# Kernel tuning notes

Hardware: AMD Instinct MI355X
Metric: run time of the kernel (lower is better)

Reference implementation:

```python
import jax, jax.numpy as jnp
import numpy as np

B, N, D = 16, 4096, 256
S = 8            # num_slots
ITERS = 3
H = 256          # mlp hidden = max(dim, 256)
SCALE = D ** -0.5
TEMP = 1.0
LN_EPS = 1e-5


def _ln(x, g, b):
    mu = jnp.mean(x, axis=-1, keepdims=True)
    var = jnp.var(x, axis=-1, keepdims=True)
    return (x - mu) * jax.lax.rsqrt(var + LN_EPS) * g + b


def setup_inputs() -> dict:
    key = jax.random.key(0)
    ks = jax.random.split(key, 16)
    xav = float(np.sqrt(6.0 / (S * D + D)))  # xavier_uniform over (1,S,D)
    lin = float(np.sqrt(1.0 / D))
    return {
        "embeddings": jax.random.normal(ks[0], (B, N, D), jnp.float32),
        "slots_noise": jax.random.normal(ks[1], (1, S, D), jnp.float32) * 0.0 + jax.random.normal(ks[1], (B, S, D), jnp.float32),
        "slots_mu": jax.random.uniform(ks[2], (1, S, D), jnp.float32, -xav, xav),
        "slots_logsigma": jax.random.uniform(ks[3], (1, S, D), jnp.float32, -xav, xav),
        "Wk": jax.random.uniform(ks[4], (S, D, D), jnp.float32, -lin, lin),
        "Wq": jax.random.uniform(ks[5], (D, D), jnp.float32, -lin, lin),
        "Wv": jax.random.uniform(ks[6], (S, D, D), jnp.float32, -lin, lin),
        "W_ih": jax.random.uniform(ks[7], (3 * D, D), jnp.float32, -lin, lin),
        "W_hh": jax.random.uniform(ks[8], (3 * D, D), jnp.float32, -lin, lin),
        "b_ih": jax.random.uniform(ks[9], (3 * D,), jnp.float32, -lin, lin),
        "b_hh": jax.random.uniform(ks[10], (3 * D,), jnp.float32, -lin, lin),
        "W1": jax.random.uniform(ks[11], (H, D), jnp.float32, -lin, lin),
        "b1": jnp.zeros((H,), jnp.float32),
        "W2": jax.random.uniform(ks[12], (D, H), jnp.float32, -float(np.sqrt(1.0 / H)), float(np.sqrt(1.0 / H))),
        "b2": jnp.zeros((D,), jnp.float32),
        "g_in": jnp.ones((D,), jnp.float32), "be_in": jnp.zeros((D,), jnp.float32),
        "g_s": jnp.ones((D,), jnp.float32), "be_s": jnp.zeros((D,), jnp.float32),
        "g_ff": jnp.ones((D,), jnp.float32), "be_ff": jnp.zeros((D,), jnp.float32),
    }


def _gru(x, h, W_ih, W_hh, b_ih, b_hh):
    # torch.nn.GRUCell math; x,h: [M, D]
    gi = x @ W_ih.T + b_ih
    gh = h @ W_hh.T + b_hh
    i_r, i_z, i_n = jnp.split(gi, 3, axis=-1)
    h_r, h_z, h_n = jnp.split(gh, 3, axis=-1)
    r = jax.nn.sigmoid(i_r + h_r)
    z = jax.nn.sigmoid(i_z + h_z)
    n = jnp.tanh(i_n + r * h_n)
    return (1.0 - z) * n + z * h


def reference(embeddings, slots_noise, slots_mu, slots_logsigma, Wk, Wq, Wv,
              W_ih, W_hh, b_ih, b_hh, W1, b1, W2, b2,
              g_in, be_in, g_s, be_s, g_ff, be_ff):
    b, n, d = embeddings.shape
    slots = slots_mu + jnp.exp(slots_logsigma) * slots_noise   # [B,S,D]
    emb = _ln(embeddings, g_in, be_in)                          # [B,N,D]
    # per-slot keys / values: keys[s] = emb @ Wk[s].T  -> [S,B,N,D]
    keys = jnp.einsum('bnd,sed->sbne', emb, Wk)
    values = jnp.einsum('bnd,sed->sbne', emb, Wv)

    attn_vis = None
    for _ in range(ITERS):
        slots_prev = slots
        slots_n = _ln(slots, g_s, be_s)
        q = jnp.einsum('bsd,ed->bse', slots_n, Wq)              # [B,S,D]
        dots = jnp.einsum('bsd,sbnd->bsn', q, keys) * SCALE     # [B,S,N]
        attn = jax.nn.softmax(dots / TEMP, axis=1)              # softmax over slots
        attn_vis = attn
        attn_w = attn / jnp.sum(attn, axis=-1, keepdims=True)   # normalize over tokens
        updates = jnp.einsum('sbnd,bsn->bsd', values, attn_w)   # [B,S,D]
        h = _gru(updates.reshape(b * S, d), slots_prev.reshape(b * S, d),
                 W_ih, W_hh, b_ih, b_hh).reshape(b, S, d)
        ff = _ln(h, g_ff, be_ff)
        slots = h + (jax.nn.relu(ff @ W1.T + b1) @ W2.T + b2)
    return slots, attn_vis
```

## Files before the change

### kernel.cpp

```cpp
#include <hip/hip_runtime.h>

#define DEVI __device__ __forceinline__

constexpr float SCALE = 0.0625f;
constexpr float LN_EPS = 1e-5f;

DEVI float dot8f(const float* __restrict__ w, const float* __restrict__ x){
  float4 a = *(const float4*)w;
  float4 b = *(const float4*)(w + 4);
  return a.x*x[0]+a.y*x[1]+a.z*x[2]+a.w*x[3]+b.x*x[4]+b.y*x[5]+b.z*x[6]+b.w*x[7];
}

DEVI float gemv256(const float* __restrict__ W, const float* __restrict__ xv,
                   float (*part)[33], int tid){
  const int c8 = tid & 31, dp = tid >> 5;
  float xs8[8];
  #pragma unroll
  for (int j = 0; j < 8; ++j) xs8[j] = xv[c8*8 + j];
  #pragma unroll 4
  for (int di = 0; di < 32; ++di){
    int d = dp*32 + di;
    part[d][c8] = dot8f(W + (size_t)d*256 + c8*8, xs8);
  }
  __syncthreads();
  float acc = 0.f;
  #pragma unroll
  for (int p = 0; p < 32; ++p) acc += part[tid][p];
  __syncthreads();
  return acc;
}

DEVI float block_ln(float x, const float* __restrict__ g, const float* __restrict__ be,
                    float* red, int tid, int lane, int wv){
  float v1 = x, v2 = x*x;
  #pragma unroll
  for (int o = 32; o; o >>= 1){ v1 += __shfl_xor(v1,o,64); v2 += __shfl_xor(v2,o,64); }
  if (lane == 0){ red[wv] = v1; red[4+wv] = v2; }
  __syncthreads();
  float mu = (red[0]+red[1]+red[2]+red[3]) * (1.f/256.f);
  float var = (red[4]+red[5]+red[6]+red[7]) * (1.f/256.f) - mu*mu;
  float inv = rsqrtf(var + LN_EPS);
  float r = (x - mu)*inv*g[tid] + be[tid];
  __syncthreads();
  return r;
}

DEVI void q_gen(float snew, int r, int s, int tid, int lane, int wv,
                const float* __restrict__ Wq, const float* __restrict__ Wk,
                const float* __restrict__ g_s, const float* __restrict__ be_s,
                const float* __restrict__ g_in, const float* __restrict__ be_in,
                float* __restrict__ qg, float* __restrict__ gqbq,
                float* xv, float (*part)[33], float (*partK)[256], float* red){
  float sn = block_ln(snew, g_s, be_s, red, tid, lane, wv);
  xv[tid] = sn; __syncthreads();
  float q = gemv256(Wq, xv, part, tid);
  xv[tid] = q; __syncthreads();
  const int c8 = tid & 31, ep = tid >> 5;
  float acc8[8];
  #pragma unroll
  for (int j = 0; j < 8; ++j) acc8[j] = 0.f;
  const float* Wb = Wk + ((size_t)s*256)*256 + c8*8;
  #pragma unroll 4
  for (int ei = 0; ei < 32; ++ei){
    int e = ep*32 + ei;
    const float* wp = Wb + (size_t)e*256;
    float4 wa = *(const float4*)wp;
    float4 wb = *(const float4*)(wp + 4);
    float qe = xv[e];
    acc8[0] += qe*wa.x; acc8[1] += qe*wa.y; acc8[2] += qe*wa.z; acc8[3] += qe*wa.w;
    acc8[4] += qe*wb.x; acc8[5] += qe*wb.y; acc8[6] += qe*wb.z; acc8[7] += qe*wb.w;
  }
  float* pk = &partK[ep][c8*8];
  #pragma unroll
  for (int j = 0; j < 8; ++j) pk[j] = acc8[j];
  __syncthreads();
  float qk = 0.f;
  #pragma unroll
  for (int p = 0; p < 8; ++p) qk += partK[p][tid];
  float qgv = qk * g_in[tid] * SCALE;
  float bqv = qk * be_in[tid] * SCALE;
  qg[r*256 + tid] = qgv;
  float vq = qgv, vb = bqv;
  #pragma unroll
  for (int o = 32; o; o >>= 1){ vq += __shfl_xor(vq,o,64); vb += __shfl_xor(vb,o,64); }
  if (lane == 0){ red[wv] = vq; red[4+wv] = vb; }
  __syncthreads();
  if (tid == 0) gqbq[r*2+0] = red[0]+red[1]+red[2]+red[3];
  if (tid == 1) gqbq[r*2+1] = red[4]+red[5]+red[6]+red[7];
}

__global__ __launch_bounds__(256) void k_qg0(const float* __restrict__ noise,
    const float* __restrict__ smu, const float* __restrict__ slsig,
    const float* __restrict__ Wq, const float* __restrict__ Wk,
    const float* __restrict__ g_s, const float* __restrict__ be_s,
    const float* __restrict__ g_in, const float* __restrict__ be_in,
    float* __restrict__ slots, float* __restrict__ qg, float* __restrict__ gqbq,
    float* __restrict__ uacc, float* __restrict__ Zacc){
  __shared__ float part[256][33];
  __shared__ float partK[8][256];
  __shared__ float xv[256];
  __shared__ float red[8];
  const int r = blockIdx.x, tid = threadIdx.x;
  const int s = r & 7, lane = tid & 63, wv = tid >> 6;
  float x = smu[s*256 + tid] + expf(slsig[s*256 + tid]) * noise[r*256 + tid];
  slots[r*256 + tid] = x;
  uacc[r*256 + tid] = 0.f;
  if (tid == 0) Zacc[r] = 0.f;
  q_gen(x, r, s, tid, lane, wv, Wq, Wk, g_s, be_s, g_in, be_in, qg, gqbq,
        xv, part, partK, red);
}

__global__ __launch_bounds__(256) void k_main(const float* __restrict__ emb,
    const float* __restrict__ qg, const float* __restrict__ gqbq,
    const float* __restrict__ g_in, const float* __restrict__ be_in,
    float* __restrict__ uacc, float* __restrict__ Zacc,
    float* __restrict__ out_attn, int write_attn){
  __shared__ float qgL[2048];
  __shared__ float aL[256], avL[256];
  __shared__ float Wred[2][8][4];
  __shared__ float Zs[8], A2s[8], GqL[8], BqL[8];

  const int tid = threadIdx.x, lane = tid & 63, wv = tid >> 6;
  const int blk = blockIdx.x, b = blk >> 7, tile = blk & 127;
  const int n0 = tile * 32;

  {
    const float4* src = (const float4*)(qg + (size_t)b * 2048);
    float4* dst = (float4*)qgL;
    #pragma unroll
    for (int k = 0; k < 2; ++k){
      int w = tid + k*256;
      int s = w >> 6, f = w & 63, qq = f >> 3, j = f & 7;
      dst[s*64 + qq*8 + ((j + qq) & 7)] = src[w];
    }
  }
  if (tid < 8){
    GqL[tid] = gqbq[(b*8 + tid)*2 + 0];
    BqL[tid] = gqbq[(b*8 + tid)*2 + 1];
  }
  __syncthreads();

  const int t = tid >> 3;
  const int qq = tid & 7;
  {
    const float4* xrow = (const float4*)(emb + ((size_t)(b*4096 + n0 + t))*256 + qq*32);
    float4 xv4[8];
    #pragma unroll
    for (int j = 0; j < 8; ++j) xv4[j] = xrow[j];
    float s1 = 0.f, s2 = 0.f, acc[8];
    #pragma unroll
    for (int s = 0; s < 8; ++s) acc[s] = 0.f;
    #pragma unroll
    for (int j = 0; j < 8; ++j){
      float4 u = xv4[j];
      s1 += (u.x+u.y)+(u.z+u.w);
      s2 += u.x*u.x+u.y*u.y+u.z*u.z+u.w*u.w;
      const float* qb = qgL + qq*32 + ((j + qq) & 7)*4;
      #pragma unroll
      for (int s = 0; s < 8; ++s){
        float4 q0 = *(const float4*)(qb + s*256);
        acc[s] += u.x*q0.x + u.y*q0.y + u.z*q0.z + u.w*q0.w;
      }
    }
    #pragma unroll
    for (int o = 1; o <= 4; o <<= 1){
      s1 += __shfl_xor(s1,o,64); s2 += __shfl_xor(s2,o,64);
      #pragma unroll
      for (int s = 0; s < 8; ++s) acc[s] += __shfl_xor(acc[s],o,64);
    }
    float mu = s1 * (1.f/256.f);
    float var = s2 * (1.f/256.f) - mu*mu;
    float inv = rsqrtf(var + LN_EPS);
    float dv[8], mx = -1e30f;
    #pragma unroll
    for (int s = 0; s < 8; ++s){
      dv[s] = inv * (acc[s] - mu * GqL[s]) + BqL[s];
      mx = fmaxf(mx, dv[s]);
    }
    float den = 0.f;
    #pragma unroll
    for (int s = 0; s < 8; ++s){ dv[s] = expf(dv[s] - mx); den += dv[s]; }
    float rden = 1.f / den;
    #pragma unroll
    for (int s = 0; s < 8; ++s){
      float at = dv[s] * rden;
      float av = at * inv;
      if (qq == 0){ avL[s*32 + t] = at; aL[s*32 + t] = av; }
      float z1 = at, z2 = av * mu;
      #pragma unroll
      for (int o = 32; o; o >>= 1){ z1 += __shfl_xor(z1, o, 64); z2 += __shfl_xor(z2, o, 64); }
      if (lane == 0){ Wred[0][s][wv] = z1 * 0.125f; Wred[1][s][wv] = z2 * 0.125f; }
    }
  }
  __syncthreads();
  if (tid < 8){
    Zs[tid]  = Wred[0][tid][0]+Wred[0][tid][1]+Wred[0][tid][2]+Wred[0][tid][3];
    A2s[tid] = Wred[1][tid][0]+Wred[1][tid][1]+Wred[1][tid][2]+Wred[1][tid][3];
  }
  if (write_attn){
    int s = tid >> 5, tk = tid & 31;
    out_attn[((size_t)(b*8 + s))*4096 + n0 + tk] = avL[s*32 + tk];
  }
  __syncthreads();
  {
    const int c = tid;
    const float* xcol = emb + ((size_t)(b*4096 + n0))*256 + c;
    float S1[8];
    #pragma unroll
    for (int s = 0; s < 8; ++s) S1[s] = 0.f;
    #pragma unroll 2
    for (int t4 = 0; t4 < 8; ++t4){
      float x0 = xcol[(t4*4+0)*256];
      float x1 = xcol[(t4*4+1)*256];
      float x2 = xcol[(t4*4+2)*256];
      float x3 = xcol[(t4*4+3)*256];
      #pragma unroll
      for (int s = 0; s < 8; ++s){
        float4 a4 = *(const float4*)(&aL[s*32 + t4*4]);
        S1[s] += x0*a4.x + x1*a4.y + x2*a4.z + x3*a4.w;
      }
    }
    float gc = g_in[c], bc = be_in[c];
    float* dst = uacc + ((size_t)b*8)*256 + c;
    #pragma unroll
    for (int s = 0; s < 8; ++s){
      atomicAdd(&dst[s*256], gc * (S1[s] - A2s[s]) + bc * Zs[s]);
    }
    if (tid < 8) atomicAdd(&Zacc[b*8 + tid], Zs[tid]);
  }
}

__global__ __launch_bounds__(256) void k_fused(
    float* __restrict__ slots, float* __restrict__ uacc, float* __restrict__ Zacc,
    const float* __restrict__ Wv,
    const float* __restrict__ W_ih, const float* __restrict__ W_hh,
    const float* __restrict__ b_ih, const float* __restrict__ b_hh,
    const float* __restrict__ W1, const float* __restrict__ b1,
    const float* __restrict__ W2, const float* __restrict__ b2,
    const float* __restrict__ g_ff, const float* __restrict__ be_ff,
    const float* __restrict__ Wq, const float* __restrict__ Wk,
    const float* __restrict__ g_s, const float* __restrict__ be_s,
    const float* __restrict__ g_in, const float* __restrict__ be_in,
    float* __restrict__ qg, float* __restrict__ gqbq,
    float* __restrict__ out_slots, int last){
  __shared__ float part[256][33];
  __shared__ float partK[8][256];
  __shared__ float xv[256];
  __shared__ float red[8];
  __shared__ float zsh;
  const int r = blockIdx.x, tid = threadIdx.x;
  const int s = r & 7, lane = tid & 63, wv = tid >> 6;

  float u = uacc[r*256 + tid];
  uacc[r*256 + tid] = 0.f;
  if (tid == 0){ zsh = Zacc[r]; Zacc[r] = 0.f; }
  xv[tid] = u;
  __syncthreads();
  const float rz = 1.f / zsh;
  float upd = gemv256(Wv + (size_t)s*65536, xv, part, tid) * rz;

  xv[tid] = upd; __syncthreads();
  float i_r = gemv256(W_ih,           xv, part, tid) + b_ih[tid];
  float i_z = gemv256(W_ih +  65536,  xv, part, tid) + b_ih[256 + tid];
  float i_n = gemv256(W_ih + 131072,  xv, part, tid) + b_ih[512 + tid];

  float hp = slots[r*256 + tid];
  xv[tid] = hp; __syncthreads();
  float h_r = gemv256(W_hh,           xv, part, tid) + b_hh[tid];
  float h_z = gemv256(W_hh +  65536,  xv, part, tid) + b_hh[256 + tid];
  float h_n = gemv256(W_hh + 131072,  xv, part, tid) + b_hh[512 + tid];

  float rg = 1.f/(1.f + expf(-(i_r + h_r)));
  float zg = 1.f/(1.f + expf(-(i_z + h_z)));
  float ng = tanhf(i_n + rg*h_n);
  float h  = (1.f - zg)*ng + zg*hp;

  float lnh = block_ln(h, g_ff, be_ff, red, tid, lane, wv);
  xv[tid] = lnh; __syncthreads();
  float hid = fmaxf(gemv256(W1, xv, part, tid) + b1[tid], 0.f);
  xv[tid] = hid; __syncthreads();
  float out = h + gemv256(W2, xv, part, tid) + b2[tid];
  slots[r*256 + tid] = out;
  if (last){
    out_slots[r*256 + tid] = out;
    return;
  }
  q_gen(out, r, s, tid, lane, wv, Wq, Wk, g_s, be_s, g_in, be_in, qg, gqbq,
        xv, part, partK, red);
}

extern "C" void kernel_launch(void* const* d_in, const int* in_sizes, int n_in,
                              void* d_out, int out_size, void* d_ws, size_t ws_size,
                              hipStream_t stream){
  const float* emb   = (const float*)d_in[0];
  const float* noise = (const float*)d_in[1];
  const float* smu   = (const float*)d_in[2];
  const float* slsig = (const float*)d_in[3];
  const float* Wk    = (const float*)d_in[4];
  const float* Wq    = (const float*)d_in[5];
  const float* Wv    = (const float*)d_in[6];
  const float* W_ih  = (const float*)d_in[7];
  const float* W_hh  = (const float*)d_in[8];
  const float* b_ih  = (const float*)d_in[9];
  const float* b_hh  = (const float*)d_in[10];
  const float* W1    = (const float*)d_in[11];
  const float* b1    = (const float*)d_in[12];
  const float* W2    = (const float*)d_in[13];
  const float* b2    = (const float*)d_in[14];
  const float* g_in  = (const float*)d_in[15];
  const float* be_in = (const float*)d_in[16];
  const float* g_s   = (const float*)d_in[17];
  const float* be_s  = (const float*)d_in[18];
  const float* g_ff  = (const float*)d_in[19];
  const float* be_ff = (const float*)d_in[20];

  float* ws    = (float*)d_ws;
  float* slots = ws;
  float* qg    = ws + 32768;
  float* gqbq  = ws + 65536;
  float* uacc  = ws + 65792;
  float* Zacc  = ws + 98560;

  float* out_slots = (float*)d_out;
  float* out_attn  = out_slots + 32768;
  const int has_attn = (out_size >= 32768 + 16*8*4096);

  k_qg0<<<dim3(128), dim3(256), 0, stream>>>(noise, smu, slsig, Wq, Wk,
      g_s, be_s, g_in, be_in, slots, qg, gqbq, uacc, Zacc);
  for (int it = 0; it < 3; ++it){
    int last = (it == 2);
    k_main<<<dim3(2048), dim3(256), 0, stream>>>(emb, qg, gqbq, g_in, be_in,
        uacc, Zacc, out_attn, last && has_attn);
    k_fused<<<dim3(128), dim3(256), 0, stream>>>(slots, uacc, Zacc, Wv,
        W_ih, W_hh, b_ih, b_hh, W1, b1, W2, b2, g_ff, be_ff,
        Wq, Wk, g_s, be_s, g_in, be_in, qg, gqbq, out_slots, last);
  }
}
```

Before: 383.2 us.

## Widen slot-update blocks to 1024 threads and double token tile in main kernel

The per-slot GRU/MLP/query kernels now run 1024-thread blocks, so each GEMV row slice is split across four times as many threads with guarded reductions. This targets the latency of the serial small-GEMV chain. The main attention kernel processes 64 tokens per block in two passes, halving the grid and the number of atomic adds to the update accumulators. Its weighted-sum step is restructured into float4 row-parallel partial sums reduced through shared memory, and the atomic target order is staggered per block to spread contention. The changes cost larger shared memory and more syncs per block.

```diff
diff --git a/kernel.cpp b/kernel.cpp
--- a/kernel.cpp
+++ b/kernel.cpp
@@ -11,58 +11,64 @@
   return a.x*x[0]+a.y*x[1]+a.z*x[2]+a.w*x[3]+b.x*x[4]+b.y*x[5]+b.z*x[6]+b.w*x[7];
 }
 
-DEVI float gemv256(const float* __restrict__ W, const float* __restrict__ xv,
-                   float (*part)[33], int tid){
+DEVI float gemv256_w(const float* __restrict__ W, const float* __restrict__ xv,
+                     float (*part)[33], int tid){
   const int c8 = tid & 31, dp = tid >> 5;
   float xs8[8];
   #pragma unroll
   for (int j = 0; j < 8; ++j) xs8[j] = xv[c8*8 + j];
-  #pragma unroll 4
-  for (int di = 0; di < 32; ++di){
-    int d = dp*32 + di;
+  #pragma unroll
+  for (int di = 0; di < 8; ++di){
+    int d = dp*8 + di;
     part[d][c8] = dot8f(W + (size_t)d*256 + c8*8, xs8);
   }
   __syncthreads();
   float acc = 0.f;
-  #pragma unroll
-  for (int p = 0; p < 32; ++p) acc += part[tid][p];
+  if (tid < 256){
+    #pragma unroll
+    for (int p = 0; p < 32; ++p) acc += part[tid][p];
+  }
   __syncthreads();
   return acc;
 }
 
-DEVI float block_ln(float x, const float* __restrict__ g, const float* __restrict__ be,
-                    float* red, int tid, int lane, int wv){
+DEVI float block_ln2(float x, const float* __restrict__ g, const float* __restrict__ be,
+                     float* red, int tid){
+  const int lane = tid & 63, wv = tid >> 6;
   float v1 = x, v2 = x*x;
   #pragma unroll
   for (int o = 32; o; o >>= 1){ v1 += __shfl_xor(v1,o,64); v2 += __shfl_xor(v2,o,64); }
-  if (lane == 0){ red[wv] = v1; red[4+wv] = v2; }
+  if (tid < 256 && lane == 0){ red[wv] = v1; red[4+wv] = v2; }
   __syncthreads();
   float mu = (red[0]+red[1]+red[2]+red[3]) * (1.f/256.f);
   float var = (red[4]+red[5]+red[6]+red[7]) * (1.f/256.f) - mu*mu;
   float inv = rsqrtf(var + LN_EPS);
-  float r = (x - mu)*inv*g[tid] + be[tid];
+  float r = 0.f;
+  if (tid < 256) r = (x - mu)*inv*g[tid] + be[tid];
   __syncthreads();
   return r;
 }
 
-DEVI void q_gen(float snew, int r, int s, int tid, int lane, int wv,
+DEVI void q_gen(float snew, int r, int s, int tid,
                 const float* __restrict__ Wq, const float* __restrict__ Wk,
                 const float* __restrict__ g_s, const float* __restrict__ be_s,
                 const float* __restrict__ g_in, const float* __restrict__ be_in,
                 float* __restrict__ qg, float* __restrict__ gqbq,
                 float* xv, float (*part)[33], float (*partK)[256], float* red){
-  float sn = block_ln(snew, g_s, be_s, red, tid, lane, wv);
-  xv[tid] = sn; __syncthreads();
-  float q = gemv256(Wq, xv, part, tid);
-  xv[tid] = q; __syncthreads();
+  float sn = block_ln2(snew, g_s, be_s, red, tid);
+  if (tid < 256) xv[tid] = sn;
+  __syncthreads();
+  float q = gemv256_w(Wq, xv, part, tid);
+  if (tid < 256) xv[tid] = q;
+  __syncthreads();
   const int c8 = tid & 31, ep = tid >> 5;
   float acc8[8];
   #pragma unroll
   for (int j = 0; j < 8; ++j) acc8[j] = 0.f;
   const float* Wb = Wk + ((size_t)s*256)*256 + c8*8;
-  #pragma unroll 4
-  for (int ei = 0; ei < 32; ++ei){
-    int e = ep*32 + ei;
+  #pragma unroll
+  for (int ei = 0; ei < 8; ++ei){
+    int e = ep*8 + ei;
     const float* wp = Wb + (size_t)e*256;
     float4 wa = *(const float4*)wp;
     float4 wb = *(const float4*)(wp + 4);
@@ -74,22 +80,25 @@
   #pragma unroll
   for (int j = 0; j < 8; ++j) pk[j] = acc8[j];
   __syncthreads();
-  float qk = 0.f;
-  #pragma unroll
-  for (int p = 0; p < 8; ++p) qk += partK[p][tid];
-  float qgv = qk * g_in[tid] * SCALE;
-  float bqv = qk * be_in[tid] * SCALE;
-  qg[r*256 + tid] = qgv;
-  float vq = qgv, vb = bqv;
+  float vq = 0.f, vb = 0.f;
+  if (tid < 256){
+    float qk = 0.f;
+    #pragma unroll
+    for (int p = 0; p < 32; ++p) qk += partK[p][tid];
+    float qgv = qk * g_in[tid] * SCALE;
+    float bqv = qk * be_in[tid] * SCALE;
+    qg[r*256 + tid] = qgv;
+    vq = qgv; vb = bqv;
+  }
   #pragma unroll
   for (int o = 32; o; o >>= 1){ vq += __shfl_xor(vq,o,64); vb += __shfl_xor(vb,o,64); }
-  if (lane == 0){ red[wv] = vq; red[4+wv] = vb; }
+  if (tid < 256 && (tid & 63) == 0){ red[tid>>6] = vq; red[4+(tid>>6)] = vb; }
   __syncthreads();
   if (tid == 0) gqbq[r*2+0] = red[0]+red[1]+red[2]+red[3];
   if (tid == 1) gqbq[r*2+1] = red[4]+red[5]+red[6]+red[7];
 }
 
-__global__ __launch_bounds__(256) void k_qg0(const float* __restrict__ noise,
+__global__ __launch_bounds__(1024) void k_qg0(const float* __restrict__ noise,
     const float* __restrict__ smu, const float* __restrict__ slsig,
     const float* __restrict__ Wq, const float* __restrict__ Wk,
     const float* __restrict__ g_s, const float* __restrict__ be_s,
@@ -97,17 +106,19 @@
     float* __restrict__ slots, float* __restrict__ qg, float* __restrict__ gqbq,
     float* __restrict__ uacc, float* __restrict__ Zacc){
   __shared__ float part[256][33];
-  __shared__ float partK[8][256];
+  __shared__ float partK[32][256];
   __shared__ float xv[256];
   __shared__ float red[8];
   const int r = blockIdx.x, tid = threadIdx.x;
-  const int s = r & 7, lane = tid & 63, wv = tid >> 6;
-  float x = smu[s*256 + tid] + expf(slsig[s*256 + tid]) * noise[r*256 + tid];
-  slots[r*256 + tid] = x;
-  uacc[r*256 + tid] = 0.f;
+  const int s = r & 7;
+  float x = 0.f;
+  if (tid < 256){
+    x = smu[s*256 + tid] + expf(slsig[s*256 + tid]) * noise[r*256 + tid];
+    slots[r*256 + tid] = x;
+    uacc[r*256 + tid] = 0.f;
+  }
   if (tid == 0) Zacc[r] = 0.f;
-  q_gen(x, r, s, tid, lane, wv, Wq, Wk, g_s, be_s, g_in, be_in, qg, gqbq,
-        xv, part, partK, red);
+  q_gen(x, r, s, tid, Wq, Wk, g_s, be_s, g_in, be_in, qg, gqbq, xv, part, partK, red);
 }
 
 __global__ __launch_bounds__(256) void k_main(const float* __restrict__ emb,
@@ -116,13 +127,14 @@
     float* __restrict__ uacc, float* __restrict__ Zacc,
     float* __restrict__ out_attn, int write_attn){
   __shared__ float qgL[2048];
-  __shared__ float aL[256], avL[256];
-  __shared__ float Wred[2][8][4];
+  __shared__ float aL[512], avL[512];
+  __shared__ float4 Sp4[4*8*64];
+  __shared__ float red2[2][8][4];
   __shared__ float Zs[8], A2s[8], GqL[8], BqL[8];
 
   const int tid = threadIdx.x, lane = tid & 63, wv = tid >> 6;
-  const int blk = blockIdx.x, b = blk >> 7, tile = blk & 127;
-  const int n0 = tile * 32;
+  const int blk = blockIdx.x, b = blk >> 6, tile = blk & 63;
+  const int n0 = tile * 64;
 
   {
     const float4* src = (const float4*)(qg + (size_t)b * 2048);
@@ -140,9 +152,14 @@
   }
   __syncthreads();
 
-  const int t = tid >> 3;
   const int qq = tid & 7;
-  {
+  float zsum[8], z2sum[8];
+  #pragma unroll
+  for (int s = 0; s < 8; ++s){ zsum[s] = 0.f; z2sum[s] = 0.f; }
+
+  #pragma unroll
+  for (int pass = 0; pass < 2; ++pass){
+    const int t = pass*32 + (tid >> 3);
     const float4* xrow = (const float4*)(emb + ((size_t)(b*4096 + n0 + t))*256 + qq*32);
     float4 xv4[8];
     #pragma unroll
@@ -185,52 +202,67 @@
     for (int s = 0; s < 8; ++s){
       float at = dv[s] * rden;
       float av = at * inv;
-      if (qq == 0){ avL[s*32 + t] = at; aL[s*32 + t] = av; }
+      if (qq == 0){ avL[s*64 + t] = at; aL[s*64 + t] = av; }
       float z1 = at, z2 = av * mu;
       #pragma unroll
       for (int o = 32; o; o >>= 1){ z1 += __shfl_xor(z1, o, 64); z2 += __shfl_xor(z2, o, 64); }
-      if (lane == 0){ Wred[0][s][wv] = z1 * 0.125f; Wred[1][s][wv] = z2 * 0.125f; }
-    }
+      zsum[s] += z1 * 0.125f;
+      z2sum[s] += z2 * 0.125f;
+    }
+  }
+  if (lane == 0){
+    #pragma unroll
+    for (int s = 0; s < 8; ++s){ red2[0][s][wv] = zsum[s]; red2[1][s][wv] = z2sum[s]; }
   }
   __syncthreads();
   if (tid < 8){
-    Zs[tid]  = Wred[0][tid][0]+Wred[0][tid][1]+Wred[0][tid][2]+Wred[0][tid][3];
-    A2s[tid] = Wred[1][tid][0]+Wred[1][tid][1]+Wred[1][tid][2]+Wred[1][tid][3];
+    Zs[tid]  = red2[0][tid][0]+red2[0][tid][1]+red2[0][tid][2]+red2[0][tid][3];
+    A2s[tid] = red2[1][tid][0]+red2[1][tid][1]+red2[1][tid][2]+red2[1][tid][3];
   }
   if (write_attn){
     int s = tid >> 5, tk = tid & 31;
-    out_attn[((size_t)(b*8 + s))*4096 + n0 + tk] = avL[s*32 + tk];
+    #pragma unroll
+    for (int p = 0; p < 2; ++p)
+      out_attn[((size_t)(b*8 + s))*4096 + n0 + p*32 + tk] = avL[s*64 + p*32 + tk];
+  }
+  __syncthreads();
+  {
+    const int r4 = tid >> 6, cq = tid & 63;
+    float4 S1[8];
+    #pragma unroll
+    for (int s = 0; s < 8; ++s) S1[s] = make_float4(0.f,0.f,0.f,0.f);
+    const float4* xbase = (const float4*)(emb + ((size_t)(b*4096 + n0))*256) + cq;
+    #pragma unroll 4
+    for (int i = 0; i < 16; ++i){
+      int t = r4 + i*4;
+      float4 x4 = xbase[t*64];
+      #pragma unroll
+      for (int s = 0; s < 8; ++s){
+        float a = aL[s*64 + t];
+        S1[s].x += a*x4.x; S1[s].y += a*x4.y; S1[s].z += a*x4.z; S1[s].w += a*x4.w;
+      }
+    }
+    #pragma unroll
+    for (int s = 0; s < 8; ++s) Sp4[(r4*8 + s)*64 + cq] = S1[s];
   }
   __syncthreads();
   {
     const int c = tid;
-    const float* xcol = emb + ((size_t)(b*4096 + n0))*256 + c;
-    float S1[8];
-    #pragma unroll
-    for (int s = 0; s < 8; ++s) S1[s] = 0.f;
-    #pragma unroll 2
-    for (int t4 = 0; t4 < 8; ++t4){
-      float x0 = xcol[(t4*4+0)*256];
-      float x1 = xcol[(t4*4+1)*256];
-      float x2 = xcol[(t4*4+2)*256];
-      float x3 = xcol[(t4*4+3)*256];
-      #pragma unroll
-      for (int s = 0; s < 8; ++s){
-        float4 a4 = *(const float4*)(&aL[s*32 + t4*4]);
-        S1[s] += x0*a4.x + x1*a4.y + x2*a4.z + x3*a4.w;
-      }
-    }
+    const float* Sp = (const float*)Sp4;
     float gc = g_in[c], bc = be_in[c];
     float* dst = uacc + ((size_t)b*8)*256 + c;
     #pragma unroll
-    for (int s = 0; s < 8; ++s){
-      atomicAdd(&dst[s*256], gc * (S1[s] - A2s[s]) + bc * Zs[s]);
+    for (int si = 0; si < 8; ++si){
+      int s = (si + blk) & 7;
+      float v = Sp[(0*8+s)*256 + c] + Sp[(1*8+s)*256 + c]
+              + Sp[(2*8+s)*256 + c] + Sp[(3*8+s)*256 + c];
+      atomicAdd(&dst[s*256], gc * (v - A2s[s]) + bc * Zs[s]);
     }
     if (tid < 8) atomicAdd(&Zacc[b*8 + tid], Zs[tid]);
   }
 }
 
-__global__ __launch_bounds__(256) void k_fused(
+__global__ __launch_bounds__(1024) void k_fused(
     float* __restrict__ slots, float* __restrict__ uacc, float* __restrict__ Zacc,
     const float* __restrict__ Wv,
     const float* __restrict__ W_ih, const float* __restrict__ W_hh,
@@ -244,49 +276,64 @@
     float* __restrict__ qg, float* __restrict__ gqbq,
     float* __restrict__ out_slots, int last){
   __shared__ float part[256][33];
-  __shared__ float partK[8][256];
+  __shared__ float partK[32][256];
   __shared__ float xv[256];
   __shared__ float red[8];
   __shared__ float zsh;
   const int r = blockIdx.x, tid = threadIdx.x;
-  const int s = r & 7, lane = tid & 63, wv = tid >> 6;
-
-  float u = uacc[r*256 + tid];
-  uacc[r*256 + tid] = 0.f;
+  const int s = r & 7;
+
+  float u = 0.f, hp = 0.f;
+  if (tid < 256){
+    u = uacc[r*256 + tid];
+    uacc[r*256 + tid] = 0.f;
+    xv[tid] = u;
+  }
   if (tid == 0){ zsh = Zacc[r]; Zacc[r] = 0.f; }
-  xv[tid] = u;
   __syncthreads();
   const float rz = 1.f / zsh;
-  float upd = gemv256(Wv + (size_t)s*65536, xv, part, tid) * rz;
-
-  xv[tid] = upd; __syncthreads();
-  float i_r = gemv256(W_ih,           xv, part, tid) + b_ih[tid];
-  float i_z = gemv256(W_ih +  65536,  xv, part, tid) + b_ih[256 + tid];
-  float i_n = gemv256(W_ih + 131072,  xv, part, tid) + b_ih[512 + tid];
-
-  float hp = slots[r*256 + tid];
-  xv[tid] = hp; __syncthreads();
-  float h_r = gemv256(W_hh,           xv, part, tid) + b_hh[tid];
-  float h_z = gemv256(W_hh +  65536,  xv, part, tid) + b_hh[256 + tid];
-  float h_n = gemv256(W_hh + 131072,  xv, part, tid) + b_hh[512 + tid];
-
-  float rg = 1.f/(1.f + expf(-(i_r + h_r)));
-  float zg = 1.f/(1.f + expf(-(i_z + h_z)));
-  float ng = tanhf(i_n + rg*h_n);
-  float h  = (1.f - zg)*ng + zg*hp;
-
-  float lnh = block_ln(h, g_ff, be_ff, red, tid, lane, wv);
-  xv[tid] = lnh; __syncthreads();
-  float hid = fmaxf(gemv256(W1, xv, part, tid) + b1[tid], 0.f);
-  xv[tid] = hid; __syncthreads();
-  float out = h + gemv256(W2, xv, part, tid) + b2[tid];
-  slots[r*256 + tid] = out;
-  if (last){
-    out_slots[r*256 + tid] = out;
-    return;
-  }
-  q_gen(out, r, s, tid, lane, wv, Wq, Wk, g_s, be_s, g_in, be_in, qg, gqbq,
-        xv, part, partK, red);
+  float upd = gemv256_w(Wv + (size_t)s*65536, xv, part, tid) * rz;
+
+  if (tid < 256) xv[tid] = upd;
+  __syncthreads();
+  float i_r = gemv256_w(W_ih,          xv, part, tid);
+  float i_z = gemv256_w(W_ih +  65536, xv, part, tid);
+  float i_n = gemv256_w(W_ih + 131072, xv, part, tid);
+
+  if (tid < 256){
+    hp = slots[r*256 + tid];
+    xv[tid] = hp;
+  }
+  __syncthreads();
+  float h_r = gemv256_w(W_hh,          xv, part, tid);
+  float h_z = gemv256_w(W_hh +  65536, xv, part, tid);
+  float h_n = gemv256_w(W_hh + 131072, xv, part, tid);
+
+  float h = 0.f;
+  if (tid < 256){
+    i_r += b_ih[tid];       h_r += b_hh[tid];
+    i_z += b_ih[256 + tid]; h_z += b_hh[256 + tid];
+    i_n += b_ih[512 + tid]; h_n += b_hh[512 + tid];
+    float rg = 1.f/(1.f + expf(-(i_r + h_r)));
+    float zg = 1.f/(1.f + expf(-(i_z + h_z)));
+    float ng = tanhf(i_n + rg*h_n);
+    h = (1.f - zg)*ng + zg*hp;
+  }
+  float lnh = block_ln2(h, g_ff, be_ff, red, tid);
+  if (tid < 256) xv[tid] = lnh;
+  __syncthreads();
+  float hid = gemv256_w(W1, xv, part, tid);
+  if (tid < 256) xv[tid] = fmaxf(hid + b1[tid], 0.f);
+  __syncthreads();
+  float o2 = gemv256_w(W2, xv, part, tid);
+  float out = 0.f;
+  if (tid < 256){
+    out = h + o2 + b2[tid];
+    slots[r*256 + tid] = out;
+    if (last) out_slots[r*256 + tid] = out;
+  }
+  if (last) return;
+  q_gen(out, r, s, tid, Wq, Wk, g_s, be_s, g_in, be_in, qg, gqbq, xv, part, partK, red);
 }
 
 extern "C" void kernel_launch(void* const* d_in, const int* in_sizes, int n_in,
@@ -325,13 +372,13 @@
   float* out_attn  = out_slots + 32768;
   const int has_attn = (out_size >= 32768 + 16*8*4096);
 
-  k_qg0<<<dim3(128), dim3(256), 0, stream>>>(noise, smu, slsig, Wq, Wk,
+  k_qg0<<<dim3(128), dim3(1024), 0, stream>>>(noise, smu, slsig, Wq, Wk,
       g_s, be_s, g_in, be_in, slots, qg, gqbq, uacc, Zacc);
   for (int it = 0; it < 3; ++it){
     int last = (it == 2);
-    k_main<<<dim3(2048), dim3(256), 0, stream>>>(emb, qg, gqbq, g_in, be_in,
+    k_main<<<dim3(1024), dim3(256), 0, stream>>>(emb, qg, gqbq, g_in, be_in,
         uacc, Zacc, out_attn, last && has_attn);
-    k_fused<<<dim3(128), dim3(256), 0, stream>>>(slots, uacc, Zacc, Wv,
+    k_fused<<<dim3(128), dim3(1024), 0, stream>>>(slots, uacc, Zacc, Wv,
         W_ih, W_hh, b_ih, b_hh, W1, b1, W2, b2, g_ff, be_ff,
         Wq, Wk, g_s, be_s, g_in, be_in, qg, gqbq, out_slots, last);
   }
```

After: 362.3 us. -5.5%, faster.
